# Kernel optimization log

Hardware: AMD Instinct MI355X
Metric: run time of the kernel (lower is better)

Reference implementation:

```python
import jax, jax.numpy as jnp
import numpy as np

B, L, D, UNITS = 2, 1024, 256, 32


def setup_inputs() -> dict:
    key = jax.random.key(0)
    k1, k2, k3, k4 = jax.random.split(key, 4)
    inputs = jax.random.normal(k1, (B, L, D), dtype=jnp.float32)
    # glorot-style scaled init for weights
    Wt = jax.random.normal(k2, (D, UNITS), dtype=jnp.float32) * (1.0 / np.sqrt(D))
    Wx = jax.random.normal(k3, (UNITS, D), dtype=jnp.float32) * (1.0 / np.sqrt(D))
    bh = jnp.zeros((UNITS,), dtype=jnp.float32)
    Wa = jax.random.normal(k4, (UNITS, 1), dtype=jnp.float32) * (1.0 / np.sqrt(UNITS))
    ba = jnp.zeros((1,), dtype=jnp.float32)
    return {"inputs": inputs, "Wt": Wt, "Wx": Wx, "bh": bh, "Wa": Wa, "ba": ba}


def reference(inputs, Wt, Wx, bh, Wa, ba):
    # q: [B, L, U], k: [B, L, U]  (Wx is stored (U, D), used transposed)
    q = jnp.einsum('bld,du->blu', inputs, Wt)
    k = jnp.einsum('bld,ud->blu', inputs, Wx)
    # beta: [B, Lq, Lk, U] broadcast-add + tanh (the big intermediate)
    beta = jnp.tanh(q[:, :, None, :] + k[:, None, :, :] + bh)
    # alpha: [B, Lq, Lk]
    alpha = jnp.einsum('bqku,u->bqk', beta, Wa[:, 0]) + ba[0]
    # numerically-stable softmax over keys (last axis)
    a = jax.nn.softmax(alpha, axis=-1)
    # weighted sum of values: [B, L, D]
    c_r = jnp.einsum('bqk,bkd->bqd', a, inputs)
    return c_r
```

## Files before the change

### kernel.cpp

```cpp
#include <hip/hip_runtime.h>
#include <cstdint>
#include <cmath>

#define B_ 2
#define L_ 1024
#define D_ 256
#define U_ 32
#define ROWS_ 2048
#define WBS 280
#define PSTR 1032

typedef __attribute__((ext_vector_type(8))) short short8;
typedef __attribute__((ext_vector_type(4))) float floatx4;

#define OFF_P  0u
#define OFF_XT (OFF_P + 524288u)
#define OFF_WV (OFF_XT + 1048576u)

__device__ __forceinline__ float bf2f(unsigned short u) {
    union { unsigned int i; float f; } v; v.i = ((unsigned int)u) << 16; return v.f;
}
__device__ __forceinline__ unsigned short f2bf(float f) {
    union { float f; unsigned int i; } v; v.f = f;
    unsigned int r = v.i + 0x7FFFu + ((v.i >> 16) & 1u);
    return (unsigned short)(r >> 16);
}
__device__ __forceinline__ unsigned int pack_bf(float a, float b) {
    union { float f; unsigned int i; } ua, ub; ua.f = a; ub.f = b;
    unsigned int ra = ua.i + 0x7FFFu + ((ua.i >> 16) & 1u);
    unsigned int rb = ub.i + 0x7FFFu + ((ub.i >> 16) & 1u);
    return (ra >> 16) | (rb & 0xFFFF0000u);
}

__device__ __forceinline__ int sniff_is_f32(const void* x) {
    const unsigned short* xu = (const unsigned short*)x;
    float f = bf2f(xu[2 * (threadIdx.x & 63)]);
    bool plausible = (f == f) && (fabsf(f) < 1e4f) && (fabsf(f) > 1e-10f);
    unsigned long long m = __ballot(plausible);
    return (__popcll(m) >= 60) ? 0 : 1;
}

__device__ __forceinline__ short8 cvt8(const float* p) {
    float4 fa = *(const float4*)p;
    float4 fb = *(const float4*)(p + 4);
    union { short8 s; unsigned int u[4]; } r;
    r.u[0] = pack_bf(fa.x, fa.y);
    r.u[1] = pack_bf(fa.z, fa.w);
    r.u[2] = pack_bf(fb.x, fb.y);
    r.u[3] = pack_bf(fb.z, fb.w);
    return r.s;
}

__global__ void proj_all(const void* __restrict__ x,  const void* __restrict__ Wt,
                         const void* __restrict__ Wx, const void* __restrict__ bh,
                         const void* __restrict__ Wa,
                         float* __restrict__ P, unsigned short* __restrict__ xT,
                         float* __restrict__ WV) {
    const int t = threadIdx.x;
    const int isf32 = sniff_is_f32(x);
    const int n0 = blockIdx.x * 32;
    const int b  = n0 >> 10;
    const int l0 = n0 & (L_ - 1);
    __shared__ unsigned short wb[64 * WBS];
    __shared__ unsigned short xtile[D_ * 34];

    if (blockIdx.x == 0 && t < U_) {
        float wav = isf32 ? ((const float*)Wa)[t] : bf2f(((const unsigned short*)Wa)[t]);
        WV[t] = -2.0f * wav;
    }

    for (int j = 0; j < 32; ++j) {
        const int i = t + 256 * j;
        unsigned short v = isf32 ? f2bf(((const float*)Wt)[i])
                                 : ((const unsigned short*)Wt)[i];
        wb[(i & 31) * WBS + (i >> 5)] = v;
    }
    for (int j = 0; j < 32; ++j) {
        const int e = t + 256 * j;
        unsigned short v = isf32 ? f2bf(((const float*)Wx)[e])
                                 : ((const unsigned short*)Wx)[e];
        wb[(32 + (e >> 8)) * WBS + (e & 255)] = v;
    }
    __syncthreads();

    const int w    = t >> 6;
    const int lane = t & 63;
    const int mt   = w & 1;
    const int rh   = w >> 1;
    const int m    = lane & 15;
    const int kho  = lane >> 4;
    const int u0   = mt * 32;
    const int row  = n0 + 16 * rh + m;

    floatx4 acc0 = {0,0,0,0}, acc1 = {0,0,0,0};
    #pragma unroll
    for (int k0 = 0; k0 < D_; k0 += 32) {
        const int ks = k0 + kho * 8;
        short8 a0 = *(const short8*)(wb + (u0 + m) * WBS + ks);
        short8 a1 = *(const short8*)(wb + (u0 + 16 + m) * WBS + ks);
        short8 b0;
        if (isf32) b0 = cvt8((const float*)x + (size_t)row * D_ + ks);
        else       b0 = *(const short8*)((const unsigned short*)x + (size_t)row * D_ + ks);
        acc0 = __builtin_amdgcn_mfma_f32_16x16x32_bf16(a0, b0, acc0, 0, 0, 0);
        acc1 = __builtin_amdgcn_mfma_f32_16x16x32_bf16(a1, b0, acc1, 0, 0, 0);
        if (mt == 0) {
            union { short8 s; unsigned short h[8]; } uu; uu.s = b0;
            #pragma unroll
            for (int jj = 0; jj < 8; ++jj)
                xtile[(ks + jj) * 34 + 16 * rh + m] = uu.h[jj];
        }
    }

    const float SC = 2.0f * 1.4426950408889634f;
    const int col = lane & 15;
    const int rb  = (lane >> 4) * 4;
    #pragma unroll
    for (int r = 0; r < 4; ++r) {
        const int ua = u0 + rb + r, ub_ = u0 + 16 + rb + r;
        float bh0 = 0.f, bh1 = 0.f;
        if (mt == 0) {
            bh0 = isf32 ? ((const float*)bh)[rb + r]      : bf2f(((const unsigned short*)bh)[rb + r]);
            bh1 = isf32 ? ((const float*)bh)[16 + rb + r] : bf2f(((const unsigned short*)bh)[16 + rb + r]);
        }
        P[(size_t)ua  * ROWS_ + n0 + 16 * rh + col] = __builtin_amdgcn_exp2f(SC * (acc0[r] + bh0));
        P[(size_t)ub_ * ROWS_ + n0 + 16 * rh + col] = __builtin_amdgcn_exp2f(SC * (acc1[r] + bh1));
    }

    __syncthreads();
    unsigned short* xtb = xT + (size_t)b * (D_ * L_) + l0;
    #pragma unroll
    for (int i = 0; i < 16; ++i) {
        const int idx = t + 256 * i;
        const int d = idx >> 4, wq = idx & 15;
        unsigned int p = *(const unsigned int*)(xtile + d * 34 + 2 * wq);
        *(unsigned int*)(xtb + (size_t)d * L_ + 2 * wq) = p;
    }
}

__global__ __launch_bounds__(512) void alpha_pv(const float* __restrict__ P,
                                                const float* __restrict__ WV,
                                                const void* __restrict__ x,
                                                const unsigned short* __restrict__ xT,
                                                void* __restrict__ out) {
    const int w    = threadIdx.x >> 6;
    const int lane = threadIdx.x & 63;
    const int row  = blockIdx.x * 8 + w;
    const int b    = row >> 10;
    const int isf32 = sniff_is_f32(x);
    __shared__ unsigned short Pl[16 * PSTR];

    const float* Pq = P + row;
    const float* kb = P + (size_t)32 * ROWS_ + (size_t)b * L_ + 4 * lane;
    float alp[16];
    #pragma unroll
    for (int j = 0; j < 16; ++j) alp[j] = 0.f;

    #pragma unroll 2
    for (int u = 0; u < U_; ++u) {
        const float equ = Pq[(size_t)u * ROWS_];
        const float wu  = WV[u];
        const float* kr = kb + (size_t)u * ROWS_;
        float4 k0 = *(const float4*)(kr);
        float4 k1 = *(const float4*)(kr + 256);
        float4 k2 = *(const float4*)(kr + 512);
        float4 k3 = *(const float4*)(kr + 768);
        alp[0]  = fmaf(wu, __builtin_amdgcn_rcpf(fmaf(equ, k0.x, 1.f)), alp[0]);
        alp[1]  = fmaf(wu, __builtin_amdgcn_rcpf(fmaf(equ, k0.y, 1.f)), alp[1]);
        alp[2]  = fmaf(wu, __builtin_amdgcn_rcpf(fmaf(equ, k0.z, 1.f)), alp[2]);
        alp[3]  = fmaf(wu, __builtin_amdgcn_rcpf(fmaf(equ, k0.w, 1.f)), alp[3]);
        alp[4]  = fmaf(wu, __builtin_amdgcn_rcpf(fmaf(equ, k1.x, 1.f)), alp[4]);
        alp[5]  = fmaf(wu, __builtin_amdgcn_rcpf(fmaf(equ, k1.y, 1.f)), alp[5]);
        alp[6]  = fmaf(wu, __builtin_amdgcn_rcpf(fmaf(equ, k1.z, 1.f)), alp[6]);
        alp[7]  = fmaf(wu, __builtin_amdgcn_rcpf(fmaf(equ, k1.w, 1.f)), alp[7]);
        alp[8]  = fmaf(wu, __builtin_amdgcn_rcpf(fmaf(equ, k2.x, 1.f)), alp[8]);
        alp[9]  = fmaf(wu, __builtin_amdgcn_rcpf(fmaf(equ, k2.y, 1.f)), alp[9]);
        alp[10] = fmaf(wu, __builtin_amdgcn_rcpf(fmaf(equ, k2.z, 1.f)), alp[10]);
        alp[11] = fmaf(wu, __builtin_amdgcn_rcpf(fmaf(equ, k2.w, 1.f)), alp[11]);
        alp[12] = fmaf(wu, __builtin_amdgcn_rcpf(fmaf(equ, k3.x, 1.f)), alp[12]);
        alp[13] = fmaf(wu, __builtin_amdgcn_rcpf(fmaf(equ, k3.y, 1.f)), alp[13]);
        alp[14] = fmaf(wu, __builtin_amdgcn_rcpf(fmaf(equ, k3.z, 1.f)), alp[14]);
        alp[15] = fmaf(wu, __builtin_amdgcn_rcpf(fmaf(equ, k3.w, 1.f)), alp[15]);
    }

    float amax = alp[0];
    #pragma unroll
    for (int j = 1; j < 16; ++j) amax = fmaxf(amax, alp[j]);
    #pragma unroll
    for (int off = 32; off > 0; off >>= 1) amax = fmaxf(amax, __shfl_xor(amax, off, 64));

    const float L2E = 1.4426950408889634f;
    float s = 0.f;
    #pragma unroll
    for (int j = 0; j < 16; ++j) {
        alp[j] = __builtin_amdgcn_exp2f((alp[j] - amax) * L2E);
        s += alp[j];
    }
    #pragma unroll
    for (int off = 32; off > 0; off >>= 1) s += __shfl_xor(s, off, 64);
    const float rinv = __builtin_amdgcn_rcpf(s);

    #pragma unroll
    for (int jj = 0; jj < 4; ++jj) {
        ushort4 pk;
        pk.x = f2bf(alp[4*jj+0] * rinv);
        pk.y = f2bf(alp[4*jj+1] * rinv);
        pk.z = f2bf(alp[4*jj+2] * rinv);
        pk.w = f2bf(alp[4*jj+3] * rinv);
        *(ushort4*)(Pl + w * PSTR + jj * 256 + 4 * lane) = pk;
    }
    __syncthreads();

    const int m  = lane & 15;
    const int ko = (lane >> 4) * 8;
    const int d0 = w * 32;
    const unsigned short* xb0 = xT + (size_t)b * (D_ * L_) + (size_t)(d0 + m) * L_ + ko;
    const unsigned short* xb1 = xb0 + (size_t)16 * L_;
    const unsigned short* pp  = Pl + (size_t)m * PSTR + ko;

    floatx4 acc0 = {0,0,0,0}, acc1 = {0,0,0,0};
    short8 pa = *(const short8*)(pp);
    short8 x0 = *(const short8*)(xb0);
    short8 x1 = *(const short8*)(xb1);
    for (int ks = 32; ks < L_; ks += 32) {
        short8 npa = *(const short8*)(pp + ks);
        short8 nx0 = *(const short8*)(xb0 + ks);
        short8 nx1 = *(const short8*)(xb1 + ks);
        acc0 = __builtin_amdgcn_mfma_f32_16x16x32_bf16(pa, x0, acc0, 0, 0, 0);
        acc1 = __builtin_amdgcn_mfma_f32_16x16x32_bf16(pa, x1, acc1, 0, 0, 0);
        pa = npa; x0 = nx0; x1 = nx1;
    }
    acc0 = __builtin_amdgcn_mfma_f32_16x16x32_bf16(pa, x0, acc0, 0, 0, 0);
    acc1 = __builtin_amdgcn_mfma_f32_16x16x32_bf16(pa, x1, acc1, 0, 0, 0);

    const int col = lane & 15;
    const int rb  = (lane >> 4) * 4;
    const int qi0 = (blockIdx.x * 8) & (L_ - 1);
    const size_t obase = (size_t)b * (L_ * D_) + (size_t)qi0 * D_;
    if (rb < 8) {
        if (isf32) {
            float* ob = (float*)out + obase;
            #pragma unroll
            for (int r = 0; r < 4; ++r) {
                ob[(size_t)(rb + r) * D_ + d0 + col]      = acc0[r];
                ob[(size_t)(rb + r) * D_ + d0 + 16 + col] = acc1[r];
            }
        } else {
            unsigned short* ob = (unsigned short*)out + obase;
            #pragma unroll
            for (int r = 0; r < 4; ++r) {
                ob[(size_t)(rb + r) * D_ + d0 + col]      = f2bf(acc0[r]);
                ob[(size_t)(rb + r) * D_ + d0 + 16 + col] = f2bf(acc1[r]);
            }
        }
    }
}

extern "C" void kernel_launch(void* const* d_in, const int* in_sizes, int n_in,
                              void* d_out, int out_size, void* d_ws, size_t ws_size,
                              hipStream_t stream) {
    const void* x  = d_in[0];
    const void* Wt = d_in[1];
    const void* Wx = d_in[2];
    const void* bh = d_in[3];
    const void* Wa = d_in[4];

    char* ws = (char*)d_ws;
    float*          P   = (float*)(ws + OFF_P);
    unsigned short* xT  = (unsigned short*)(ws + OFF_XT);
    float*          WV  = (float*)(ws + OFF_WV);

    proj_all<<<ROWS_ / 32, 256, 0, stream>>>(x, Wt, Wx, bh, Wa, P, xT, WV);
    alpha_pv<<<ROWS_ / 8, 512, 0, stream>>>(P, WV, x, xT, d_out);
}
```

Measured before the change: 113.4 us.

## Replace MFMA projection with fp32 FMA over smaller row tiles; shuffle per-unit scalars

The projection kernel now computes q/k in fp32 with scalar FMAs from shared memory instead of bf16 MFMA. It uses 8 rows per block with 512 threads, launching 256 blocks instead of 64, so more of the GPU is busy. Each block reloads the full 64 KB fp32 weight matrix, which raises redundant global traffic and shared-memory use. In alpha_pv, the per-unit query exponent and weight are loaded once per lane and broadcast with wave shuffles instead of per-iteration global loads, and the loop unroll goes from 2 to 4.

```diff
diff --git a/kernel.cpp b/kernel.cpp
--- a/kernel.cpp
+++ b/kernel.cpp
@@ -7,7 +7,7 @@
 #define D_ 256
 #define U_ 32
 #define ROWS_ 2048
-#define WBS 280
+#define WBSTR 65
 #define PSTR 1032
 
 typedef __attribute__((ext_vector_type(8))) short short8;
@@ -24,12 +24,6 @@
     union { float f; unsigned int i; } v; v.f = f;
     unsigned int r = v.i + 0x7FFFu + ((v.i >> 16) & 1u);
     return (unsigned short)(r >> 16);
-}
-__device__ __forceinline__ unsigned int pack_bf(float a, float b) {
-    union { float f; unsigned int i; } ua, ub; ua.f = a; ub.f = b;
-    unsigned int ra = ua.i + 0x7FFFu + ((ua.i >> 16) & 1u);
-    unsigned int rb = ub.i + 0x7FFFu + ((ub.i >> 16) & 1u);
-    return (ra >> 16) | (rb & 0xFFFF0000u);
 }
 
 __device__ __forceinline__ int sniff_is_f32(const void* x) {
@@ -40,100 +34,84 @@
     return (__popcll(m) >= 60) ? 0 : 1;
 }
 
-__device__ __forceinline__ short8 cvt8(const float* p) {
-    float4 fa = *(const float4*)p;
-    float4 fb = *(const float4*)(p + 4);
-    union { short8 s; unsigned int u[4]; } r;
-    r.u[0] = pack_bf(fa.x, fa.y);
-    r.u[1] = pack_bf(fa.z, fa.w);
-    r.u[2] = pack_bf(fb.x, fb.y);
-    r.u[3] = pack_bf(fb.z, fb.w);
-    return r.s;
-}
-
-__global__ void proj_all(const void* __restrict__ x,  const void* __restrict__ Wt,
+__global__ __launch_bounds__(512) void proj_all(const void* __restrict__ x,  const void* __restrict__ Wt,
                          const void* __restrict__ Wx, const void* __restrict__ bh,
                          const void* __restrict__ Wa,
                          float* __restrict__ P, unsigned short* __restrict__ xT,
                          float* __restrict__ WV) {
     const int t = threadIdx.x;
     const int isf32 = sniff_is_f32(x);
-    const int n0 = blockIdx.x * 32;
+    const int n0 = blockIdx.x * 8;
     const int b  = n0 >> 10;
     const int l0 = n0 & (L_ - 1);
-    __shared__ unsigned short wb[64 * WBS];
-    __shared__ unsigned short xtile[D_ * 34];
+    __shared__ float WB[256 * WBSTR];
+    __shared__ float XR[8 * 256];
+    __shared__ float PL[64 * 9];
 
     if (blockIdx.x == 0 && t < U_) {
         float wav = isf32 ? ((const float*)Wa)[t] : bf2f(((const unsigned short*)Wa)[t]);
         WV[t] = -2.0f * wav;
     }
 
-    for (int j = 0; j < 32; ++j) {
-        const int i = t + 256 * j;
-        unsigned short v = isf32 ? f2bf(((const float*)Wt)[i])
-                                 : ((const unsigned short*)Wt)[i];
-        wb[(i & 31) * WBS + (i >> 5)] = v;
-    }
-    for (int j = 0; j < 32; ++j) {
-        const int e = t + 256 * j;
-        unsigned short v = isf32 ? f2bf(((const float*)Wx)[e])
-                                 : ((const unsigned short*)Wx)[e];
-        wb[(32 + (e >> 8)) * WBS + (e & 255)] = v;
-    }
-    __syncthreads();
+    #pragma unroll
+    for (int j = 0; j < 16; ++j) {
+        const int i = t + 512 * j;
+        float v = isf32 ? ((const float*)Wt)[i] : bf2f(((const unsigned short*)Wt)[i]);
+        WB[(i >> 5) * WBSTR + (i & 31)] = v;
+    }
+    #pragma unroll
+    for (int j = 0; j < 16; ++j) {
+        const int e = t + 512 * j;
+        float v = isf32 ? ((const float*)Wx)[e] : bf2f(((const unsigned short*)Wx)[e]);
+        WB[(e & 255) * WBSTR + 32 + (e >> 8)] = v;
+    }
 
     const int w    = t >> 6;
     const int lane = t & 63;
-    const int mt   = w & 1;
-    const int rh   = w >> 1;
-    const int m    = lane & 15;
-    const int kho  = lane >> 4;
-    const int u0   = mt * 32;
-    const int row  = n0 + 16 * rh + m;
-
-    floatx4 acc0 = {0,0,0,0}, acc1 = {0,0,0,0};
-    #pragma unroll
-    for (int k0 = 0; k0 < D_; k0 += 32) {
-        const int ks = k0 + kho * 8;
-        short8 a0 = *(const short8*)(wb + (u0 + m) * WBS + ks);
-        short8 a1 = *(const short8*)(wb + (u0 + 16 + m) * WBS + ks);
-        short8 b0;
-        if (isf32) b0 = cvt8((const float*)x + (size_t)row * D_ + ks);
-        else       b0 = *(const short8*)((const unsigned short*)x + (size_t)row * D_ + ks);
-        acc0 = __builtin_amdgcn_mfma_f32_16x16x32_bf16(a0, b0, acc0, 0, 0, 0);
-        acc1 = __builtin_amdgcn_mfma_f32_16x16x32_bf16(a1, b0, acc1, 0, 0, 0);
-        if (mt == 0) {
-            union { short8 s; unsigned short h[8]; } uu; uu.s = b0;
-            #pragma unroll
-            for (int jj = 0; jj < 8; ++jj)
-                xtile[(ks + jj) * 34 + 16 * rh + m] = uu.h[jj];
-        }
-    }
+    const int row  = n0 + w;
+
+    if (isf32) {
+        float4 xv = *((const float4*)x + (size_t)row * (D_ / 4) + lane);
+        *(float4*)(XR + w * 256 + 4 * lane) = xv;
+    } else {
+        const unsigned short* xs = (const unsigned short*)x + (size_t)row * D_ + 4 * lane;
+        float4 xv; xv.x = bf2f(xs[0]); xv.y = bf2f(xs[1]); xv.z = bf2f(xs[2]); xv.w = bf2f(xs[3]);
+        *(float4*)(XR + w * 256 + 4 * lane) = xv;
+    }
+    __syncthreads();
+
+    float a0 = 0.f, a1 = 0.f, a2 = 0.f, a3 = 0.f;
+    const float* wbp = WB + lane;
+    const float* xr  = XR + w * 256;
+    #pragma unroll
+    for (int d = 0; d < D_; d += 4) {
+        float4 xv = *(const float4*)(xr + d);
+        a0 = fmaf(wbp[(d + 0) * WBSTR], xv.x, a0);
+        a1 = fmaf(wbp[(d + 1) * WBSTR], xv.y, a1);
+        a2 = fmaf(wbp[(d + 2) * WBSTR], xv.z, a2);
+        a3 = fmaf(wbp[(d + 3) * WBSTR], xv.w, a3);
+    }
+    float dotv = (a0 + a1) + (a2 + a3);
+
+    float bhv = 0.f;
+    if (lane < U_)
+        bhv = isf32 ? ((const float*)bh)[lane] : bf2f(((const unsigned short*)bh)[lane]);
 
     const float SC = 2.0f * 1.4426950408889634f;
-    const int col = lane & 15;
-    const int rb  = (lane >> 4) * 4;
-    #pragma unroll
-    for (int r = 0; r < 4; ++r) {
-        const int ua = u0 + rb + r, ub_ = u0 + 16 + rb + r;
-        float bh0 = 0.f, bh1 = 0.f;
-        if (mt == 0) {
-            bh0 = isf32 ? ((const float*)bh)[rb + r]      : bf2f(((const unsigned short*)bh)[rb + r]);
-            bh1 = isf32 ? ((const float*)bh)[16 + rb + r] : bf2f(((const unsigned short*)bh)[16 + rb + r]);
-        }
-        P[(size_t)ua  * ROWS_ + n0 + 16 * rh + col] = __builtin_amdgcn_exp2f(SC * (acc0[r] + bh0));
-        P[(size_t)ub_ * ROWS_ + n0 + 16 * rh + col] = __builtin_amdgcn_exp2f(SC * (acc1[r] + bh1));
-    }
-
+    PL[lane * 9 + w] = __builtin_amdgcn_exp2f(SC * (dotv + bhv));
     __syncthreads();
-    unsigned short* xtb = xT + (size_t)b * (D_ * L_) + l0;
-    #pragma unroll
-    for (int i = 0; i < 16; ++i) {
-        const int idx = t + 256 * i;
-        const int d = idx >> 4, wq = idx & 15;
-        unsigned int p = *(const unsigned int*)(xtile + d * 34 + 2 * wq);
-        *(unsigned int*)(xtb + (size_t)d * L_ + 2 * wq) = p;
+
+    {
+        const int u = t >> 3, r = t & 7;
+        P[(size_t)u * ROWS_ + n0 + r] = PL[u * 9 + r];
+    }
+
+    if (t < 256) {
+        const int d = t;
+        union { short8 s; unsigned short h[8]; } o;
+        #pragma unroll
+        for (int r = 0; r < 8; ++r) o.h[r] = f2bf(XR[r * 256 + d]);
+        *(short8*)(xT + (size_t)b * (D_ * L_) + (size_t)d * L_ + l0) = o.s;
     }
 }
 
@@ -151,14 +129,21 @@
 
     const float* Pq = P + row;
     const float* kb = P + (size_t)32 * ROWS_ + (size_t)b * L_ + 4 * lane;
+
+    float eq_l = 0.f, wu_l = 0.f;
+    if (lane < U_) {
+        eq_l = Pq[(size_t)lane * ROWS_];
+        wu_l = WV[lane];
+    }
+
     float alp[16];
     #pragma unroll
     for (int j = 0; j < 16; ++j) alp[j] = 0.f;
 
-    #pragma unroll 2
+    #pragma unroll 4
     for (int u = 0; u < U_; ++u) {
-        const float equ = Pq[(size_t)u * ROWS_];
-        const float wu  = WV[u];
+        const float equ = __shfl(eq_l, u, 64);
+        const float wu  = __shfl(wu_l, u, 64);
         const float* kr = kb + (size_t)u * ROWS_;
         float4 k0 = *(const float4*)(kr);
         float4 k1 = *(const float4*)(kr + 256);
@@ -269,6 +254,6 @@
     unsigned short* xT  = (unsigned short*)(ws + OFF_XT);
     float*          WV  = (float*)(ws + OFF_WV);
 
-    proj_all<<<ROWS_ / 32, 256, 0, stream>>>(x, Wt, Wx, bh, Wa, P, xT, WV);
+    proj_all<<<ROWS_ / 8, 512, 0, stream>>>(x, Wt, Wx, bh, Wa, P, xT, WV);
     alpha_pv<<<ROWS_ / 8, 512, 0, stream>>>(P, WV, x, xT, d_out);
 }
```

Result: slower. 163.4 us (+44.1%).

## Stage key exponentials in LDS shared across waves for alpha computation

Applied to the files above, without the earlier changes.

Loads the key-side factor rows into shared memory in two halves of 16 units so all 8 waves in a block reuse them, replacing per-wave global/L2 loads. Per-row query factors and weights are loaded once per lane and broadcast with shuffles. The P tile buffer is halved to 8 rows with MFMA rows aliased via m&7. The large LDS footprint reduces occupancy and adds block-wide barriers.

```diff
diff --git a/kernel.cpp b/kernel.cpp
--- a/kernel.cpp
+++ b/kernel.cpp
@@ -142,44 +142,66 @@
                                                 const void* __restrict__ x,
                                                 const unsigned short* __restrict__ xT,
                                                 void* __restrict__ out) {
-    const int w    = threadIdx.x >> 6;
-    const int lane = threadIdx.x & 63;
+    const int t    = threadIdx.x;
+    const int w    = t >> 6;
+    const int lane = t & 63;
     const int row  = blockIdx.x * 8 + w;
     const int b    = row >> 10;
     const int isf32 = sniff_is_f32(x);
-    __shared__ unsigned short Pl[16 * PSTR];
-
-    const float* Pq = P + row;
-    const float* kb = P + (size_t)32 * ROWS_ + (size_t)b * L_ + 4 * lane;
+    __shared__ float EK[16 * 1024];
+    __shared__ unsigned short Pl[8 * PSTR];
+
+    const float* Pq  = P + row;
+    const float* ekg = P + (size_t)32 * ROWS_ + (size_t)b * L_;
+
+    float eq_l = 0.f, wu_l = 0.f;
+    if (lane < U_) {
+        eq_l = Pq[(size_t)lane * ROWS_];
+        wu_l = WV[lane];
+    }
+
     float alp[16];
     #pragma unroll
     for (int j = 0; j < 16; ++j) alp[j] = 0.f;
 
-    #pragma unroll 2
-    for (int u = 0; u < U_; ++u) {
-        const float equ = Pq[(size_t)u * ROWS_];
-        const float wu  = WV[u];
-        const float* kr = kb + (size_t)u * ROWS_;
-        float4 k0 = *(const float4*)(kr);
-        float4 k1 = *(const float4*)(kr + 256);
-        float4 k2 = *(const float4*)(kr + 512);
-        float4 k3 = *(const float4*)(kr + 768);
-        alp[0]  = fmaf(wu, __builtin_amdgcn_rcpf(fmaf(equ, k0.x, 1.f)), alp[0]);
-        alp[1]  = fmaf(wu, __builtin_amdgcn_rcpf(fmaf(equ, k0.y, 1.f)), alp[1]);
-        alp[2]  = fmaf(wu, __builtin_amdgcn_rcpf(fmaf(equ, k0.z, 1.f)), alp[2]);
-        alp[3]  = fmaf(wu, __builtin_amdgcn_rcpf(fmaf(equ, k0.w, 1.f)), alp[3]);
-        alp[4]  = fmaf(wu, __builtin_amdgcn_rcpf(fmaf(equ, k1.x, 1.f)), alp[4]);
-        alp[5]  = fmaf(wu, __builtin_amdgcn_rcpf(fmaf(equ, k1.y, 1.f)), alp[5]);
-        alp[6]  = fmaf(wu, __builtin_amdgcn_rcpf(fmaf(equ, k1.z, 1.f)), alp[6]);
-        alp[7]  = fmaf(wu, __builtin_amdgcn_rcpf(fmaf(equ, k1.w, 1.f)), alp[7]);
-        alp[8]  = fmaf(wu, __builtin_amdgcn_rcpf(fmaf(equ, k2.x, 1.f)), alp[8]);
-        alp[9]  = fmaf(wu, __builtin_amdgcn_rcpf(fmaf(equ, k2.y, 1.f)), alp[9]);
-        alp[10] = fmaf(wu, __builtin_amdgcn_rcpf(fmaf(equ, k2.z, 1.f)), alp[10]);
-        alp[11] = fmaf(wu, __builtin_amdgcn_rcpf(fmaf(equ, k2.w, 1.f)), alp[11]);
-        alp[12] = fmaf(wu, __builtin_amdgcn_rcpf(fmaf(equ, k3.x, 1.f)), alp[12]);
-        alp[13] = fmaf(wu, __builtin_amdgcn_rcpf(fmaf(equ, k3.y, 1.f)), alp[13]);
-        alp[14] = fmaf(wu, __builtin_amdgcn_rcpf(fmaf(equ, k3.z, 1.f)), alp[14]);
-        alp[15] = fmaf(wu, __builtin_amdgcn_rcpf(fmaf(equ, k3.w, 1.f)), alp[15]);
+    for (int h = 0; h < 2; ++h) {
+        __syncthreads();
+        #pragma unroll
+        for (int j = 0; j < 8; ++j) {
+            const int idx = t + 512 * j;
+            const int ul = idx >> 8, k4 = idx & 255;
+            float4 v = *(const float4*)(ekg + (size_t)(16 * h + ul) * ROWS_ + 4 * k4);
+            *(float4*)(EK + ul * 1024 + 4 * k4) = v;
+        }
+        __syncthreads();
+
+        #pragma unroll 4
+        for (int ul = 0; ul < 16; ++ul) {
+            const int u = 16 * h + ul;
+            const float equ = __shfl(eq_l, u, 64);
+            const float wu  = __shfl(wu_l, u, 64);
+            const float* kr = EK + ul * 1024 + 4 * lane;
+            float4 k0 = *(const float4*)(kr);
+            float4 k1 = *(const float4*)(kr + 256);
+            float4 k2 = *(const float4*)(kr + 512);
+            float4 k3 = *(const float4*)(kr + 768);
+            alp[0]  = fmaf(wu, __builtin_amdgcn_rcpf(fmaf(equ, k0.x, 1.f)), alp[0]);
+            alp[1]  = fmaf(wu, __builtin_amdgcn_rcpf(fmaf(equ, k0.y, 1.f)), alp[1]);
+            alp[2]  = fmaf(wu, __builtin_amdgcn_rcpf(fmaf(equ, k0.z, 1.f)), alp[2]);
+            alp[3]  = fmaf(wu, __builtin_amdgcn_rcpf(fmaf(equ, k0.w, 1.f)), alp[3]);
+            alp[4]  = fmaf(wu, __builtin_amdgcn_rcpf(fmaf(equ, k1.x, 1.f)), alp[4]);
+            alp[5]  = fmaf(wu, __builtin_amdgcn_rcpf(fmaf(equ, k1.y, 1.f)), alp[5]);
+            alp[6]  = fmaf(wu, __builtin_amdgcn_rcpf(fmaf(equ, k1.z, 1.f)), alp[6]);
+            alp[7]  = fmaf(wu, __builtin_amdgcn_rcpf(fmaf(equ, k1.w, 1.f)), alp[7]);
+            alp[8]  = fmaf(wu, __builtin_amdgcn_rcpf(fmaf(equ, k2.x, 1.f)), alp[8]);
+            alp[9]  = fmaf(wu, __builtin_amdgcn_rcpf(fmaf(equ, k2.y, 1.f)), alp[9]);
+            alp[10] = fmaf(wu, __builtin_amdgcn_rcpf(fmaf(equ, k2.z, 1.f)), alp[10]);
+            alp[11] = fmaf(wu, __builtin_amdgcn_rcpf(fmaf(equ, k2.w, 1.f)), alp[11]);
+            alp[12] = fmaf(wu, __builtin_amdgcn_rcpf(fmaf(equ, k3.x, 1.f)), alp[12]);
+            alp[13] = fmaf(wu, __builtin_amdgcn_rcpf(fmaf(equ, k3.y, 1.f)), alp[13]);
+            alp[14] = fmaf(wu, __builtin_amdgcn_rcpf(fmaf(equ, k3.z, 1.f)), alp[14]);
+            alp[15] = fmaf(wu, __builtin_amdgcn_rcpf(fmaf(equ, k3.w, 1.f)), alp[15]);
+        }
     }
 
     float amax = alp[0];
@@ -215,7 +237,7 @@
     const int d0 = w * 32;
     const unsigned short* xb0 = xT + (size_t)b * (D_ * L_) + (size_t)(d0 + m) * L_ + ko;
     const unsigned short* xb1 = xb0 + (size_t)16 * L_;
-    const unsigned short* pp  = Pl + (size_t)m * PSTR + ko;
+    const unsigned short* pp  = Pl + (size_t)(m & 7) * PSTR + ko;
 
     floatx4 acc0 = {0,0,0,0}, acc1 = {0,0,0,0};
     short8 pa = *(const short8*)(pp);
```

Result: no change. 112.6 us (-0.7%).
